# Optimization experiments

Measured on AMD Instinct MI355X. Metric: run time of the kernel, lower is better.

The kernel has to match this reference:

```python
import jax, jax.numpy as jnp
import numpy as np

E = 11      # num_experts
K = 6       # active_experts
P = 64      # prototype_dim
NH = 4      # attention heads
HD = P // NH


def setup_inputs() -> dict:
    key = jax.random.key(0)
    ks = jax.random.split(key, 24)
    B, C, H, W = 8, 128, 64, 64
    hid = 4 * C
    s = lambda k, shape, sc=0.02: jax.random.normal(k, shape, dtype=jnp.float32) * sc
    # orthogonal-ish prototypes via QR
    q, _ = jnp.linalg.qr(jax.random.normal(ks[1], (P, P), dtype=jnp.float32))
    return {
        "x": jax.random.normal(ks[0], (B, C, H, W), dtype=jnp.float32),
        "proto": q[:E, :],                       # (E, P)
        "ctx_w": s(ks[2], (P, C)), "ctx_b": jnp.zeros((P,), jnp.float32),
        "inp_w": s(ks[3], (P, C)), "inp_b": jnp.zeros((P,), jnp.float32),
        "wq": s(ks[4], (P, P)), "bq": jnp.zeros((P,), jnp.float32),
        "wk": s(ks[5], (P, P)), "bk": jnp.zeros((P,), jnp.float32),
        "wv": s(ks[6], (P, P)), "bv": jnp.zeros((P,), jnp.float32),
        "wo": s(ks[7], (P, P)), "bo": jnp.zeros((P,), jnp.float32),
        "ln_g": jnp.ones((P,), jnp.float32), "ln_b": jnp.zeros((P,), jnp.float32),
        "ew1": s(ks[8], (E, hid, C)), "eb1": jnp.zeros((E, hid), jnp.float32),
        "ew2": s(ks[9], (E, C, hid)), "eb2": jnp.zeros((E, C), jnp.float32),
    }


def _layernorm(x, g, b, eps=1e-5):
    m = x.mean(-1, keepdims=True)
    v = ((x - m) ** 2).mean(-1, keepdims=True)
    return (x - m) * jax.lax.rsqrt(v + eps) * g + b


def _forward(x, proto, ctx_w, ctx_b, inp_w, inp_b,
             wq, bq, wk, bk, wv, bv, wo, bo, ln_g, ln_b,
             ew1, eb1, ew2, eb2):
    B, C, H, W = x.shape
    # --- router: global context + prototype interaction ---
    gc = jnp.einsum("bchw->bc", x) / (H * W)          # (B, C) mean over HW
    gc = gc @ ctx_w.T + ctx_b                          # (B, P)
    seq = jnp.concatenate([gc[:, None, :],
                           jnp.broadcast_to(proto[None], (B, E, P))], axis=1)  # (B, E+1, P)
    S = E + 1
    q = (seq @ wq.T + bq).reshape(B, S, NH, HD)
    k = (seq @ wk.T + bk).reshape(B, S, NH, HD)
    v = (seq @ wv.T + bv).reshape(B, S, NH, HD)
    att = jax.nn.softmax(jnp.einsum("bqhd,bkhd->bhqk", q, k) / jnp.sqrt(jnp.float32(HD)), axis=-1)
    ao = jnp.einsum("bhqk,bkhd->bqhd", att, v).reshape(B, S, P) @ wo.T + bo
    seq2 = _layernorm(ao + seq, ln_g, ln_b)
    up = seq2[:, 1:, :]                                # (B, E, P) updated prototypes
    # --- per-pixel routing logits ---
    xr = jnp.einsum("bchw,pc->bphw", x, inp_w) + inp_b[None, :, None, None]
    logits = jnp.einsum("bphw,bep->behw", xr, up) / jnp.sqrt(jnp.float32(P))
    probs = jax.nn.softmax(logits, axis=1)             # (B, E, H, W)
    pt = probs.transpose(0, 2, 3, 1)                   # (B, H, W, E)
    tv, ti = jax.lax.top_k(pt, K)                      # (B, H, W, K)
    tv = tv / tv.sum(-1, keepdims=True)
    oh = jax.nn.one_hot(ti, E, dtype=x.dtype)          # (B, H, W, K, E)
    mask = (oh * tv[..., None]).sum(-2)                # (B, H, W, E) scatter of routing weights
    # --- dense expert loop with per-pixel masking ---
    final = jnp.zeros_like(x)
    for e in range(E):
        h = jax.nn.gelu(jnp.einsum("bchw,oc->bohw", x, ew1[e]) + eb1[e][None, :, None, None],
                        approximate=False)
        y = jnp.einsum("bohw,co->bchw", h, ew2[e]) + eb2[e][None, :, None, None]
        final = final + mask[..., e][:, None, :, :] * y
    # --- aux losses ---
    mean_prob = probs.mean((0, 2, 3))                  # (E,)
    mean_load = oh.sum(-2).mean((0, 1, 2))             # (E,)
    aux = E * jnp.sum(mean_prob * mean_load)
    pn = proto / jnp.linalg.norm(proto, axis=1, keepdims=True)
    corr = pn @ pn.T
    ortho = jnp.linalg.norm(corr - jnp.eye(E, dtype=x.dtype))
    return x + final, aux + 0.5 * ortho


def reference(x, proto, ctx_w, ctx_b, inp_w, inp_b,
              wq, bq, wk, bk, wv, bv, wo, bo, ln_g, ln_b,
              ew1, eb1, ew2, eb2):
    return _forward(x, proto, ctx_w, ctx_b, inp_w, inp_b,
                    wq, bq, wk, bk, wv, bv, wo, bo, ln_g, ln_b,
                    ew1, eb1, ew2, eb2)
```

## Files before the change

### kernel.cpp

```cpp
#include <hip/hip_runtime.h>

#define NE 11
#define NP 64
#define NC 128
#define NHW 4096
#define NHID 512

typedef __attribute__((ext_vector_type(8))) __bf16 bf16x8;
typedef __attribute__((ext_vector_type(4))) __bf16 bf16x4;
typedef __attribute__((ext_vector_type(4))) float f32x4;

#if __has_builtin(__builtin_amdgcn_exp2f)
#define FEXP2(x) __builtin_amdgcn_exp2f(x)
#else
#define FEXP2(x) exp2f(x)
#endif
#if __has_builtin(__builtin_amdgcn_rcpf)
#define FRCP(x) __builtin_amdgcn_rcpf(x)
#else
#define FRCP(x) (1.0f / (x))
#endif

__device__ __forceinline__ unsigned short f2bf(float f) {
    return __builtin_bit_cast(unsigned short, (__bf16)f);
}

__device__ __forceinline__ float gelu_erf(float v) {
    float av = fabsf(v);
    float z = av * 0.70710678118654752440f;
    float t = FRCP(fmaf(z, 0.3275911f, 1.0f));
    float p = t * fmaf(t, fmaf(t, fmaf(t, fmaf(t, 1.061405429f, -1.453152027f),
                                       1.421413741f), -0.284496736f), 0.254829592f);
    float e = FEXP2(z * z * -1.44269504088896f);
    float erfz = fmaf(-p, e, 1.0f);
    float hv = 0.5f * av;
    float g = fmaf(hv, erfz, hv);
    return g + fminf(v, 0.0f);
}

__device__ __forceinline__ bf16x8 ldsB(const char* base, int row, int col) {
    int off = ((row << 8) + (col << 1)) ^ ((row & 7) << 4);
    return *(const bf16x8*)(base + off);
}

__global__ void k_prep(const float* __restrict__ ew1, const float* __restrict__ ew2,
                       unsigned short* __restrict__ o1, unsigned short* __restrict__ o2,
                       const float* __restrict__ x, float* __restrict__ gc) {
    if (blockIdx.x < 512) {
        const int n = NE * NHID * NC;
        for (int i = blockIdx.x * 256 + threadIdx.x; i < n; i += 512 * 256) {
            o1[i] = f2bf(ew1[i]);
            o2[i] = f2bf(ew2[i]);
        }
    } else {
        int row = blockIdx.x - 512;
        const float* p = x + (size_t)row * NHW;
        float s = 0.f;
        for (int i = threadIdx.x; i < NHW; i += 256) s += p[i];
        __shared__ float red[256];
        red[threadIdx.x] = s;
        __syncthreads();
        for (int off = 128; off > 0; off >>= 1) {
            if (threadIdx.x < off) red[threadIdx.x] += red[threadIdx.x + off];
            __syncthreads();
        }
        if (threadIdx.x == 0) gc[row] = red[0] * (1.0f / 4096.0f);
    }
}

__global__ void k_attn(const float* __restrict__ gc, const float* __restrict__ proto,
                       const float* __restrict__ ctx_w, const float* __restrict__ ctx_b,
                       const float* __restrict__ wq, const float* __restrict__ bq,
                       const float* __restrict__ wk, const float* __restrict__ bk,
                       const float* __restrict__ wv, const float* __restrict__ bv,
                       const float* __restrict__ wo, const float* __restrict__ bo,
                       const float* __restrict__ lng, const float* __restrict__ lnb,
                       float* __restrict__ up, float* __restrict__ ortho, float* __restrict__ stats) {
    int t = threadIdx.x;
    __shared__ float seq[12][64], qs[12][64], ks_[12][64], vs[12][64], ao[12][64], rr[12][64];
    __shared__ float nr[NE], sq[NE * NE];

    if (blockIdx.x == 8) {
        if (t < 22) stats[t] = 0.0f;
        if (t < NE) {
            float s = 0.f;
            for (int p = 0; p < NP; p++) { float v = proto[t * NP + p]; s += v * v; }
            nr[t] = rsqrtf(s);
        }
        __syncthreads();
        if (t < NE * NE) {
            int i = t / NE, j = t % NE;
            float d = 0.f;
            for (int p = 0; p < NP; p++) d += proto[i * NP + p] * proto[j * NP + p];
            float c = d * nr[i] * nr[j] - (i == j ? 1.0f : 0.0f);
            sq[t] = c * c;
        }
        __syncthreads();
        if (t == 0) {
            float s = 0.f;
            for (int i = 0; i < NE * NE; i++) s += sq[i];
            *ortho = sqrtf(s);
        }
        return;
    }

    int b = blockIdx.x;
    if (t < NP) {
        float a = ctx_b[t];
        for (int c = 0; c < NC; c++) a = fmaf(gc[b * NC + c], ctx_w[t * NC + c], a);
        seq[0][t] = a;
    }
    for (int i = t; i < NE * NP; i += 256) { int e = i >> 6, p = i & 63; seq[e + 1][p] = proto[e * NP + p]; }
    __syncthreads();
    for (int i = t; i < 12 * NP; i += 256) {
        int s = i >> 6, p = i & 63;
        float aq = bq[p], ak = bk[p], av = bv[p];
        for (int pp = 0; pp < NP; pp++) {
            float sv = seq[s][pp];
            aq = fmaf(sv, wq[p * NP + pp], aq);
            ak = fmaf(sv, wk[p * NP + pp], ak);
            av = fmaf(sv, wv[p * NP + pp], av);
        }
        qs[s][p] = aq; ks_[s][p] = ak; vs[s][p] = av;
    }
    __syncthreads();
    if (t < 48) {
        int h = t / 12, qq = t % 12;
        float sc[12], m = -1e30f;
        for (int kk = 0; kk < 12; kk++) {
            float s = 0.f;
            for (int d = 0; d < 16; d++) s = fmaf(qs[qq][h * 16 + d], ks_[kk][h * 16 + d], s);
            s *= 0.25f;
            sc[kk] = s;
            if (s > m) m = s;
        }
        float den = 0.f;
        for (int kk = 0; kk < 12; kk++) { sc[kk] = expf(sc[kk] - m); den += sc[kk]; }
        float inv = 1.0f / den;
        for (int d = 0; d < 16; d++) {
            float a = 0.f;
            for (int kk = 0; kk < 12; kk++) a = fmaf(sc[kk], vs[kk][h * 16 + d], a);
            ao[qq][h * 16 + d] = a * inv;
        }
    }
    __syncthreads();
    for (int i = t; i < 12 * NP; i += 256) {
        int s = i >> 6, p = i & 63;
        float a = bo[p];
        for (int pp = 0; pp < NP; pp++) a = fmaf(ao[s][pp], wo[p * NP + pp], a);
        rr[s][p] = a + seq[s][p];
    }
    __syncthreads();
    if (t < 12) {
        int s = t;
        float m = 0.f;
        for (int p = 0; p < NP; p++) m += rr[s][p];
        m *= (1.0f / 64.0f);
        float v = 0.f;
        for (int p = 0; p < NP; p++) { float d = rr[s][p] - m; v += d * d; }
        v *= (1.0f / 64.0f);
        float is = rsqrtf(v + 1e-5f);
        if (s >= 1)
            for (int p = 0; p < NP; p++)
                up[(b * NE + s - 1) * NP + p] = (rr[s][p] - m) * is * lng[p] + lnb[p];
    }
}

__global__ __launch_bounds__(512, 4) void k_main(
    const float* __restrict__ x, const float* __restrict__ inp_w, const float* __restrict__ inp_b,
    const unsigned short* __restrict__ ew1b, const float* __restrict__ eb1,
    const unsigned short* __restrict__ ew2b, const float* __restrict__ eb2,
    const float* __restrict__ upw, float* __restrict__ stats, float* __restrict__ out) {
    int tid = threadIdx.x;
    int bimg = blockIdx.x >> 6;
    int pix0 = (blockIdx.x & 63) << 6;
    int wid = tid >> 6;
    int l15 = tid & 15;
    int l4 = (tid >> 4) & 3;

    __shared__ __align__(16) char smem[54784];
    char* xs = smem;
    float* stage = (float*)(smem + 32768);
    float* lpart = (float*)(smem + 36864);
    float* upl = (float*)(smem + 49152);
    float* wm = (float*)(smem + 51968);

    for (int i = tid; i < NE * NP; i += 512) upl[i] = upw[bimg * (NE * NP) + i];
    int pg = wid & 3;
    int pixl = tid & 63;
    float xr[16];
#pragma unroll
    for (int p = 0; p < 16; p++) xr[p] = inp_b[pg * 16 + p];

    for (int cb = 0; cb < NC; cb += 16) {
        for (int i = tid; i < 16 * 64; i += 512) {
            int cc = i >> 6, px = i & 63;
            float v = x[(size_t)(bimg * NC + cb + cc) * NHW + pix0 + px];
            stage[cc * 64 + px] = v;
            int off = ((px << 8) + ((cb + cc) << 1)) ^ ((px & 7) << 4);
            *(unsigned short*)(xs + off) = f2bf(v);
        }
        __syncthreads();
        if (tid < 256) {
#pragma unroll 4
            for (int cc = 0; cc < 16; cc++) {
                float xv = stage[cc * 64 + pixl];
#pragma unroll
                for (int p = 0; p < 16; p++)
                    xr[p] = fmaf(inp_w[(pg * 16 + p) * NC + cb + cc], xv, xr[p]);
            }
        }
        __syncthreads();
    }
    if (tid < 256) {
#pragma unroll
        for (int e = 0; e < NE; e++) {
            float a = 0.f;
#pragma unroll
            for (int p = 0; p < 16; p++) a = fmaf(upl[e * NP + pg * 16 + p], xr[p], a);
            lpart[(pg * NE + e) * 64 + pixl] = a;
        }
    }
    __syncthreads();

    if (tid < 64) {
        float pr[NE];
        float mx = -1e30f;
#pragma unroll
        for (int e = 0; e < NE; e++) {
            float l = (lpart[(0 * NE + e) * 64 + tid] + lpart[(1 * NE + e) * 64 + tid] +
                       lpart[(2 * NE + e) * 64 + tid] + lpart[(3 * NE + e) * 64 + tid]) * 0.125f;
            pr[e] = l;
            mx = fmaxf(mx, l);
        }
        float den = 0.f;
#pragma unroll
        for (int e = 0; e < NE; e++) { pr[e] = __expf(pr[e] - mx); den += pr[e]; }
        float inv = 1.0f / den;
#pragma unroll
        for (int e = 0; e < NE; e++) pr[e] *= inv;
        unsigned used = 0;
        float tvsum = 0.f;
        for (int k = 0; k < 6; k++) {
            float bv = -1.f;
            int best = 0;
#pragma unroll
            for (int e = 0; e < NE; e++) {
                bool sel = !((used >> e) & 1) && (pr[e] > bv);
                bv = sel ? pr[e] : bv;
                best = sel ? e : best;
            }
            used |= 1u << best;
            tvsum += bv;
        }
        float itv = 1.0f / tvsum;
#pragma unroll
        for (int e = 0; e < NE; e++)
            wm[e * 64 + tid] = ((used >> e) & 1) ? pr[e] * itv : 0.0f;
#pragma unroll
        for (int e = 0; e < NE; e++) {
            float s = pr[e];
            for (int off = 32; off; off >>= 1) s += __shfl_xor(s, off);
            unsigned long long bal = __ballot((used >> e) & 1);
            if (tid == 0) {
                atomicAdd(&stats[e], s);
                atomicAdd(&stats[NE + e], (float)__popcll(bal));
            }
        }
    }
    __syncthreads();

    f32x4 acc2[4];
#pragma unroll
    for (int nt = 0; nt < 4; nt++) acc2[nt] = {0.f, 0.f, 0.f, 0.f};

    for (int e = 0; e < NE; e++) {
#pragma unroll 2
        for (int j = 0; j < 4; j++) {
            char* hsbuf = (j & 1) ? (smem + 32768) : (smem + 16384);
            const unsigned short* w1p = ew1b + (size_t)(e * NHID + j * 128 + wid * 16 + l15) * NC;
            bf16x8 a1[4];
#pragma unroll
            for (int ksp = 0; ksp < 4; ksp++) a1[ksp] = *(const bf16x8*)(w1p + ksp * 32 + l4 * 8);
            f32x4 acc1[4];
#pragma unroll
            for (int nt = 0; nt < 4; nt++) acc1[nt] = {0.f, 0.f, 0.f, 0.f};
#pragma unroll
            for (int nt = 0; nt < 4; nt++)
#pragma unroll
                for (int ksp = 0; ksp < 4; ksp++) {
                    bf16x8 xb = ldsB(xs, nt * 16 + l15, ksp * 32 + l4 * 8);
                    acc1[nt] = __builtin_amdgcn_mfma_f32_16x16x32_bf16(a1[ksp], xb, acc1[nt], 0, 0, 0);
                }
            const unsigned short* w2p = ew2b + (size_t)(e * NC + wid * 16 + l15) * NHID + j * 128;
            bf16x8 a2[4];
#pragma unroll
            for (int ksp = 0; ksp < 4; ksp++) a2[ksp] = *(const bf16x8*)(w2p + ksp * 32 + l4 * 8);
            f32x4 b1 = *(const f32x4*)(eb1 + e * NHID + j * 128 + wid * 16 + l4 * 4);
            int oloc2 = (wid * 16 + l4 * 4) << 1;
#pragma unroll
            for (int nt = 0; nt < 4; nt++) {
                int px = nt * 16 + l15;
                float w = wm[e * 64 + px];
                bf16x4 hb;
#pragma unroll
                for (int r = 0; r < 4; r++) {
                    float v = acc1[nt][r] + b1[r];
                    hb[r] = (__bf16)(gelu_erf(v) * w);
                }
                int off = ((px << 8) + oloc2) ^ ((px & 7) << 4);
                *(uint2*)(hsbuf + off) = __builtin_bit_cast(uint2, hb);
            }
            __syncthreads();
#pragma unroll
            for (int nt = 0; nt < 4; nt++)
#pragma unroll
                for (int ksp = 0; ksp < 4; ksp++) {
                    bf16x8 hb2 = ldsB(hsbuf, nt * 16 + l15, ksp * 32 + l4 * 8);
                    acc2[nt] = __builtin_amdgcn_mfma_f32_16x16x32_bf16(a2[ksp], hb2, acc2[nt], 0, 0, 0);
                }
        }
    }

#pragma unroll
    for (int e = 0; e < NE; e++) {
        f32x4 b2 = *(const f32x4*)(eb2 + e * NC + wid * 16 + l4 * 4);
#pragma unroll
        for (int nt = 0; nt < 4; nt++) {
            float w = wm[e * 64 + nt * 16 + l15];
#pragma unroll
            for (int r = 0; r < 4; r++) acc2[nt][r] = fmaf(w, b2[r], acc2[nt][r]);
        }
    }
    int c0 = wid * 16 + l4 * 4;
#pragma unroll
    for (int nt = 0; nt < 4; nt++) {
        int px = pix0 + nt * 16 + l15;
#pragma unroll
        for (int r = 0; r < 4; r++) {
            size_t g = (size_t)(bimg * NC + c0 + r) * NHW + px;
            out[g] = x[g] + acc2[nt][r];
        }
    }
}

__global__ void k_final(const float* __restrict__ stats, const float* __restrict__ ortho,
                        float* __restrict__ out) {
    if (threadIdx.x == 0 && blockIdx.x == 0) {
        float aux = 0.f;
        for (int e = 0; e < NE; e++)
            aux += (stats[e] * (1.0f / 32768.0f)) * (stats[NE + e] * (1.0f / 32768.0f));
        aux *= (float)NE;
        out[4194304] = aux + 0.5f * (*ortho);
    }
}

extern "C" void kernel_launch(void* const* d_in, const int* in_sizes, int n_in,
                              void* d_out, int out_size, void* d_ws, size_t ws_size,
                              hipStream_t stream) {
    const float* x = (const float*)d_in[0];
    const float* proto = (const float*)d_in[1];
    const float* ctx_w = (const float*)d_in[2];
    const float* ctx_b = (const float*)d_in[3];
    const float* inp_w = (const float*)d_in[4];
    const float* inp_b = (const float*)d_in[5];
    const float* wq = (const float*)d_in[6];
    const float* bq = (const float*)d_in[7];
    const float* wk = (const float*)d_in[8];
    const float* bk = (const float*)d_in[9];
    const float* wv = (const float*)d_in[10];
    const float* bv = (const float*)d_in[11];
    const float* wo = (const float*)d_in[12];
    const float* bo = (const float*)d_in[13];
    const float* lng = (const float*)d_in[14];
    const float* lnb = (const float*)d_in[15];
    const float* ew1 = (const float*)d_in[16];
    const float* eb1 = (const float*)d_in[17];
    const float* ew2 = (const float*)d_in[18];
    const float* eb2 = (const float*)d_in[19];
    float* out = (float*)d_out;
    float* ws = (float*)d_ws;

    float* gc = ws;
    float* up = ws + 1024;
    float* ortho = ws + 6656;
    float* stats = ws + 6657;
    unsigned short* ew1b = (unsigned short*)(ws + 8192);
    unsigned short* ew2b = ew1b + NE * NHID * NC;

    k_prep<<<1536, 256, 0, stream>>>(ew1, ew2, ew1b, ew2b, x, gc);
    k_attn<<<9, 256, 0, stream>>>(gc, proto, ctx_w, ctx_b, wq, bq, wk, bk, wv, bv, wo, bo, lng, lnb,
                                  up, ortho, stats);
    k_main<<<512, 512, 0, stream>>>(x, inp_w, inp_b, ew1b, eb1, ew2b, eb2, up, stats, out);
    k_final<<<1, 64, 0, stream>>>(stats, ortho, out);
}
```

Before: 456.9 us.

## Keep expert hidden activations in registers via lane shuffles, split hidden dim across waves

Restructures the main expert MLP kernel to use 256 threads. Each pair of waves owns 32 pixels and splits the hidden dimension in half. The first GEMM's outputs are rearranged into the second GEMM's B-operand layout with cross-lane shuffles instead of a shared-memory round trip plus barrier per hidden chunk. The x fragments are kept in registers for the whole expert loop, and the two half-hidden partial sums are reduced through shared memory at the end. This removes the per-chunk syncthreads and LDS traffic, at the cost of many more accumulator registers (8x2 f32x4) and fewer threads per block, which may lower occupancy.

```diff
diff --git a/kernel.cpp b/kernel.cpp
--- a/kernel.cpp
+++ b/kernel.cpp
@@ -166,7 +166,7 @@
     }
 }
 
-__global__ __launch_bounds__(512, 4) void k_main(
+__global__ __launch_bounds__(256, 2) void k_main(
     const float* __restrict__ x, const float* __restrict__ inp_w, const float* __restrict__ inp_b,
     const unsigned short* __restrict__ ew1b, const float* __restrict__ eb1,
     const unsigned short* __restrict__ ew2b, const float* __restrict__ eb2,
@@ -175,25 +175,29 @@
     int bimg = blockIdx.x >> 6;
     int pix0 = (blockIdx.x & 63) << 6;
     int wid = tid >> 6;
+    int lane = tid & 63;
     int l15 = tid & 15;
     int l4 = (tid >> 4) & 3;
-
-    __shared__ __align__(16) char smem[54784];
+    int ws = wid & 1;
+    int pgrp = wid >> 1;
+    int wpx0 = pgrp << 5;
+
+    __shared__ __align__(16) char smem[41472];
     char* xs = smem;
-    float* stage = (float*)(smem + 32768);
-    float* lpart = (float*)(smem + 36864);
-    float* upl = (float*)(smem + 49152);
-    float* wm = (float*)(smem + 51968);
-
-    for (int i = tid; i < NE * NP; i += 512) upl[i] = upw[bimg * (NE * NP) + i];
-    int pg = wid & 3;
+    float* stage = (float*)(smem + 16384);
+    float* lpart = (float*)(smem + 24576);
+    float* upl = (float*)(smem + 35840);
+    float* wm = (float*)(smem + 38656);
+
+    for (int i = tid; i < NE * NP; i += 256) upl[i] = upw[bimg * (NE * NP) + i];
+    int pg = wid;
     int pixl = tid & 63;
     float xr[16];
 #pragma unroll
     for (int p = 0; p < 16; p++) xr[p] = inp_b[pg * 16 + p];
 
-    for (int cb = 0; cb < NC; cb += 16) {
-        for (int i = tid; i < 16 * 64; i += 512) {
+    for (int cb = 0; cb < NC; cb += 32) {
+        for (int i = tid; i < 32 * 64; i += 256) {
             int cc = i >> 6, px = i & 63;
             float v = x[(size_t)(bimg * NC + cb + cc) * NHW + pix0 + px];
             stage[cc * 64 + px] = v;
@@ -201,25 +205,21 @@
             *(unsigned short*)(xs + off) = f2bf(v);
         }
         __syncthreads();
-        if (tid < 256) {
 #pragma unroll 4
-            for (int cc = 0; cc < 16; cc++) {
-                float xv = stage[cc * 64 + pixl];
-#pragma unroll
-                for (int p = 0; p < 16; p++)
-                    xr[p] = fmaf(inp_w[(pg * 16 + p) * NC + cb + cc], xv, xr[p]);
-            }
+        for (int cc = 0; cc < 32; cc++) {
+            float xv = stage[cc * 64 + pixl];
+#pragma unroll
+            for (int p = 0; p < 16; p++)
+                xr[p] = fmaf(inp_w[(pg * 16 + p) * NC + cb + cc], xv, xr[p]);
         }
         __syncthreads();
     }
-    if (tid < 256) {
-#pragma unroll
-        for (int e = 0; e < NE; e++) {
-            float a = 0.f;
-#pragma unroll
-            for (int p = 0; p < 16; p++) a = fmaf(upl[e * NP + pg * 16 + p], xr[p], a);
-            lpart[(pg * NE + e) * 64 + pixl] = a;
-        }
+#pragma unroll
+    for (int e = 0; e < NE; e++) {
+        float a = 0.f;
+#pragma unroll
+        for (int p = 0; p < 16; p++) a = fmaf(upl[e * NP + pg * 16 + p], xr[p], a);
+        lpart[(pg * NE + e) * 64 + pixl] = a;
     }
     __syncthreads();
 
@@ -270,77 +270,144 @@
     }
     __syncthreads();
 
-    f32x4 acc2[4];
-#pragma unroll
-    for (int nt = 0; nt < 4; nt++) acc2[nt] = {0.f, 0.f, 0.f, 0.f};
+    bf16x8 xb[2][4];
+#pragma unroll
+    for (int nt = 0; nt < 2; nt++)
+#pragma unroll
+        for (int ksp = 0; ksp < 4; ksp++)
+            xb[nt][ksp] = ldsB(xs, wpx0 + nt * 16 + l15, ksp * 32 + l4 * 8);
+
+    int sA = l15 + 16 * (2 * (l4 & 1));
+    int sB = sA + 16;
+    bool hi = (l4 >= 2);
+
+    f32x4 acc2[8][2];
+#pragma unroll
+    for (int ct = 0; ct < 8; ct++)
+#pragma unroll
+        for (int nt = 0; nt < 2; nt++) acc2[ct][nt] = {0.f, 0.f, 0.f, 0.f};
 
     for (int e = 0; e < NE; e++) {
-#pragma unroll 2
-        for (int j = 0; j < 4; j++) {
-            char* hsbuf = (j & 1) ? (smem + 32768) : (smem + 16384);
-            const unsigned short* w1p = ew1b + (size_t)(e * NHID + j * 128 + wid * 16 + l15) * NC;
-            bf16x8 a1[4];
-#pragma unroll
-            for (int ksp = 0; ksp < 4; ksp++) a1[ksp] = *(const bf16x8*)(w1p + ksp * 32 + l4 * 8);
-            f32x4 acc1[4];
-#pragma unroll
-            for (int nt = 0; nt < 4; nt++) acc1[nt] = {0.f, 0.f, 0.f, 0.f};
-#pragma unroll
-            for (int nt = 0; nt < 4; nt++)
-#pragma unroll
-                for (int ksp = 0; ksp < 4; ksp++) {
-                    bf16x8 xb = ldsB(xs, nt * 16 + l15, ksp * 32 + l4 * 8);
-                    acc1[nt] = __builtin_amdgcn_mfma_f32_16x16x32_bf16(a1[ksp], xb, acc1[nt], 0, 0, 0);
+        float wg[2];
+        wg[0] = wm[e * 64 + wpx0 + l15];
+        wg[1] = wm[e * 64 + wpx0 + 16 + l15];
+        const unsigned short* w1e = ew1b + (size_t)e * NHID * NC;
+        const unsigned short* w2e = ew2b + (size_t)e * NC * NHID;
+        const float* b1e = eb1 + e * NHID;
+        for (int obl = 0; obl < 8; obl++) {
+            int o0 = (ws * 8 + obl) * 32;
+            bf16x8 a1[2][4];
+#pragma unroll
+            for (int m = 0; m < 2; m++)
+#pragma unroll
+                for (int ksp = 0; ksp < 4; ksp++)
+                    a1[m][ksp] = *(const bf16x8*)(w1e + (size_t)(o0 + m * 16 + l15) * NC + ksp * 32 + l4 * 8);
+            f32x4 acc1[2][2];
+#pragma unroll
+            for (int m = 0; m < 2; m++)
+#pragma unroll
+                for (int nt = 0; nt < 2; nt++) acc1[m][nt] = {0.f, 0.f, 0.f, 0.f};
+#pragma unroll
+            for (int m = 0; m < 2; m++)
+#pragma unroll
+                for (int nt = 0; nt < 2; nt++)
+#pragma unroll
+                    for (int ksp = 0; ksp < 4; ksp++)
+                        acc1[m][nt] = __builtin_amdgcn_mfma_f32_16x16x32_bf16(a1[m][ksp], xb[nt][ksp],
+                                                                              acc1[m][nt], 0, 0, 0);
+            f32x4 b1[2];
+#pragma unroll
+            for (int m = 0; m < 2; m++) b1[m] = *(const f32x4*)(b1e + o0 + m * 16 + l4 * 4);
+            uint2 pk[2][2];
+#pragma unroll
+            for (int nt = 0; nt < 2; nt++)
+#pragma unroll
+                for (int m = 0; m < 2; m++) {
+                    bf16x4 hb;
+#pragma unroll
+                    for (int r = 0; r < 4; r++)
+                        hb[r] = (__bf16)(gelu_erf(acc1[m][nt][r] + b1[m][r]) * wg[nt]);
+                    pk[nt][m] = __builtin_bit_cast(uint2, hb);
                 }
-            const unsigned short* w2p = ew2b + (size_t)(e * NC + wid * 16 + l15) * NHID + j * 128;
-            bf16x8 a2[4];
-#pragma unroll
-            for (int ksp = 0; ksp < 4; ksp++) a2[ksp] = *(const bf16x8*)(w2p + ksp * 32 + l4 * 8);
-            f32x4 b1 = *(const f32x4*)(eb1 + e * NHID + j * 128 + wid * 16 + l4 * 4);
-            int oloc2 = (wid * 16 + l4 * 4) << 1;
-#pragma unroll
-            for (int nt = 0; nt < 4; nt++) {
-                int px = nt * 16 + l15;
-                float w = wm[e * 64 + px];
-                bf16x4 hb;
+            bf16x8 hbf[2];
+#pragma unroll
+            for (int nt = 0; nt < 2; nt++) {
+                unsigned a0a = __shfl((int)pk[nt][0].x, sA);
+                unsigned a1a = __shfl((int)pk[nt][0].y, sA);
+                unsigned a0b = __shfl((int)pk[nt][0].x, sB);
+                unsigned a1b = __shfl((int)pk[nt][0].y, sB);
+                unsigned b0a = __shfl((int)pk[nt][1].x, sA);
+                unsigned b1a = __shfl((int)pk[nt][1].y, sA);
+                unsigned b0b = __shfl((int)pk[nt][1].x, sB);
+                unsigned b1b = __shfl((int)pk[nt][1].y, sB);
+                uint4 q;
+                q.x = hi ? b0a : a0a;
+                q.y = hi ? b1a : a1a;
+                q.z = hi ? b0b : a0b;
+                q.w = hi ? b1b : a1b;
+                hbf[nt] = __builtin_bit_cast(bf16x8, q);
+            }
+            bf16x8 a2f[8];
+#pragma unroll
+            for (int ct = 0; ct < 8; ct++)
+                a2f[ct] = *(const bf16x8*)(w2e + (size_t)(ct * 16 + l15) * NHID + o0 + l4 * 8);
+#pragma unroll
+            for (int ct = 0; ct < 8; ct++)
+#pragma unroll
+                for (int nt = 0; nt < 2; nt++)
+                    acc2[ct][nt] = __builtin_amdgcn_mfma_f32_16x16x32_bf16(a2f[ct], hbf[nt],
+                                                                           acc2[ct][nt], 0, 0, 0);
+        }
+    }
+
+    float* scr = (float*)(smem + pgrp * 16384);
+    __syncthreads();
+    if (ws == 1) {
+#pragma unroll
+        for (int ct = 0; ct < 8; ct++)
+#pragma unroll
+            for (int nt = 0; nt < 2; nt++) {
+                int off = (((ct * 2 + nt) * 16) ^ ((lane & 7) << 4)) >> 2;
+                *(f32x4*)(scr + lane * 64 + off) = acc2[ct][nt];
+            }
+    }
+    __syncthreads();
+    if (ws == 0) {
+#pragma unroll
+        for (int ct = 0; ct < 8; ct++)
+#pragma unroll
+            for (int nt = 0; nt < 2; nt++) {
+                int off = (((ct * 2 + nt) * 16) ^ ((lane & 7) << 4)) >> 2;
+                f32x4 o = *(const f32x4*)(scr + lane * 64 + off);
+#pragma unroll
+                for (int r = 0; r < 4; r++) acc2[ct][nt][r] += o[r];
+            }
+#pragma unroll
+        for (int e = 0; e < NE; e++) {
+            float wg0 = wm[e * 64 + wpx0 + l15];
+            float wg1 = wm[e * 64 + wpx0 + 16 + l15];
+#pragma unroll
+            for (int ct = 0; ct < 8; ct++) {
+                f32x4 b2 = *(const f32x4*)(eb2 + e * NC + ct * 16 + l4 * 4);
 #pragma unroll
                 for (int r = 0; r < 4; r++) {
-                    float v = acc1[nt][r] + b1[r];
-                    hb[r] = (__bf16)(gelu_erf(v) * w);
+                    acc2[ct][0][r] = fmaf(wg0, b2[r], acc2[ct][0][r]);
+                    acc2[ct][1][r] = fmaf(wg1, b2[r], acc2[ct][1][r]);
                 }
-                int off = ((px << 8) + oloc2) ^ ((px & 7) << 4);
-                *(uint2*)(hsbuf + off) = __builtin_bit_cast(uint2, hb);
-            }
-            __syncthreads();
-#pragma unroll
-            for (int nt = 0; nt < 4; nt++)
-#pragma unroll
-                for (int ksp = 0; ksp < 4; ksp++) {
-                    bf16x8 hb2 = ldsB(hsbuf, nt * 16 + l15, ksp * 32 + l4 * 8);
-                    acc2[nt] = __builtin_amdgcn_mfma_f32_16x16x32_bf16(a2[ksp], hb2, acc2[nt], 0, 0, 0);
+            }
+        }
+#pragma unroll
+        for (int ct = 0; ct < 8; ct++)
+#pragma unroll
+            for (int nt = 0; nt < 2; nt++) {
+                int px = pix0 + wpx0 + nt * 16 + l15;
+#pragma unroll
+                for (int r = 0; r < 4; r++) {
+                    int c = ct * 16 + l4 * 4 + r;
+                    size_t g = (size_t)(bimg * NC + c) * NHW + px;
+                    out[g] = x[g] + acc2[ct][nt][r];
                 }
-        }
-    }
-
-#pragma unroll
-    for (int e = 0; e < NE; e++) {
-        f32x4 b2 = *(const f32x4*)(eb2 + e * NC + wid * 16 + l4 * 4);
-#pragma unroll
-        for (int nt = 0; nt < 4; nt++) {
-            float w = wm[e * 64 + nt * 16 + l15];
-#pragma unroll
-            for (int r = 0; r < 4; r++) acc2[nt][r] = fmaf(w, b2[r], acc2[nt][r]);
-        }
-    }
-    int c0 = wid * 16 + l4 * 4;
-#pragma unroll
-    for (int nt = 0; nt < 4; nt++) {
-        int px = pix0 + nt * 16 + l15;
-#pragma unroll
-        for (int r = 0; r < 4; r++) {
-            size_t g = (size_t)(bimg * NC + c0 + r) * NHW + px;
-            out[g] = x[g] + acc2[nt][r];
-        }
+            }
     }
 }
 
@@ -391,6 +458,6 @@
     k_prep<<<1536, 256, 0, stream>>>(ew1, ew2, ew1b, ew2b, x, gc);
     k_attn<<<9, 256, 0, stream>>>(gc, proto, ctx_w, ctx_b, wq, bq, wk, bk, wv, bv, wo, bo, lng, lnb,
                                   up, ortho, stats);
-    k_main<<<512, 512, 0, stream>>>(x, inp_w, inp_b, ew1b, eb1, ew2b, eb2, up, stats, out);
+    k_main<<<512, 256, 0, stream>>>(x, inp_w, inp_b, ew1b, eb1, ew2b, eb2, up, stats, out);
     k_final<<<1, 64, 0, stream>>>(stats, ortho, out);
 }
```

New measurement: 590.7 us. +29.3%, slower.
